# Performance work log

Measured on AMD Instinct MI355X. Metric: run time of the kernel, lower is better.

Reference implementation:

```python
import jax, jax.numpy as jnp
import numpy as np

D_MODEL = 1024
D_INNER = 2048   # expand * d_model
D_STATE = 16
DT_RANK = 64     # ceil(d_model / 16)
D_CONV = 4
L = 2048
EPS = 1e-5


def setup_inputs() -> dict:
    key = jax.random.key(0)
    ks = jax.random.split(key, 8)
    sc = lambda k, shape: jax.random.normal(k, shape, jnp.float32) * 0.02
    A = jnp.tile(jnp.arange(1, D_STATE + 1, dtype=jnp.float32), (D_INNER, 1))
    return {
        "x": jax.random.normal(ks[0], (L, D_MODEL), jnp.float32),
        "W_in": sc(ks[1], (D_MODEL, 2 * D_INNER)),          # in_proj (no bias)
        "W_conv": sc(ks[2], (D_CONV, D_INNER)),             # depthwise conv kernel
        "b_conv": jnp.zeros((D_INNER,), jnp.float32),
        "W_x": sc(ks[3], (D_INNER, DT_RANK + 2 * D_STATE)), # x_proj (no bias)
        "W_dt": sc(ks[4], (DT_RANK, D_INNER)),
        "b_dt": jnp.zeros((D_INNER,), jnp.float32),
        "A_log": jnp.log(A),
        "D": jnp.ones((D_INNER,), jnp.float32),
        "W_out": sc(ks[5], (D_INNER, D_MODEL)),             # out_proj (no bias)
        "ln_scale": jnp.ones((D_MODEL,), jnp.float32),
        "ln_bias": jnp.zeros((D_MODEL,), jnp.float32),
        "drop_key": 0,  # unused: training=False -> DropPath is identity
    }


def reference(x, W_in, W_conv, b_conv, W_x, W_dt, b_dt, A_log, D, W_out,
              ln_scale, ln_bias, drop_key):
    l = x.shape[0]
    # LayerNorm (flax default: mean/var over features)
    mu = jnp.mean(x, axis=-1, keepdims=True)
    var = jnp.mean(jnp.square(x), axis=-1, keepdims=True) - jnp.square(mu)
    xn = (x - mu) * jax.lax.rsqrt(var + EPS) * ln_scale + ln_bias

    # MambaBlock
    xr = xn @ W_in                         # (l, 2*d_inner)
    u, res = xr[:, :D_INNER], xr[:, D_INNER:]

    # causal depthwise conv: pad left d_conv-1, take first l outputs
    up = jnp.pad(u, ((D_CONV - 1, 0), (0, 0)))
    uc = b_conv + sum(up[k:k + l] * W_conv[k] for k in range(D_CONV))
    u2 = jax.nn.silu(uc)                   # (l, d_inner)

    # SSM params (input-dependent)
    x_dbl = u2 @ W_x                       # (l, dt_rank + 2n)
    dt = x_dbl[:, :DT_RANK]
    B = x_dbl[:, DT_RANK:DT_RANK + D_STATE]
    C = x_dbl[:, DT_RANK + D_STATE:]
    delta = jax.nn.softplus(dt @ W_dt + b_dt)   # (l, d_inner)
    A = -jnp.exp(A_log)                         # (d_inner, n)

    dA = jnp.exp(jnp.einsum('ld,dn->ldn', delta, A))   # (l, d_inner, n)
    dBu = jnp.einsum('ld,ln->ldn', delta * u2, B)       # (l, d_inner, n)

    def step(h, inp):
        dA_t, dBu_t, C_t = inp
        h = dA_t * h + dBu_t               # (d_inner, n)
        return h, h @ C_t                  # y_t: (d_inner,)

    h0 = jnp.zeros((D_INNER, D_STATE), dtype=u2.dtype)
    _, ys = jax.lax.scan(step, h0, (dA, dBu, C))
    y = ys + u2 * D                        # (l, d_inner)

    y = y * jax.nn.silu(res)
    out = y @ W_out                        # (l, d_model)
    return out + x                         # residual (DropPath identity in eval)
```

## Files before the change

### kernel.cpp

```cpp
#include <hip/hip_runtime.h>
#include <math.h>

#define L_SEQ 2048
#define DM 1024
#define DI 2048
#define DS 16
#define DTR 64
#define EPS 1e-5f
#define NSEG 16
#define SEGLEN 128

typedef float f32x4 __attribute__((ext_vector_type(4)));
typedef __bf16 bf16x8 __attribute__((ext_vector_type(8)));
typedef _Float16 h16x2 __attribute__((ext_vector_type(2)));

static __device__ __forceinline__ unsigned short f2bf(float f) {
  union { float f; unsigned u; } v; v.f = f;
  unsigned r = v.u + 0x7fffu + ((v.u >> 16) & 1u);
  return (unsigned short)(r >> 16);
}
static __device__ __forceinline__ float bf2f(unsigned short s) {
  union { unsigned u; float f; } v; v.u = ((unsigned)s) << 16;
  return v.f;
}

static __device__ __forceinline__ void gload16(const void* g, void* l) {
  __builtin_amdgcn_global_load_lds(
      (__attribute__((address_space(1))) void*)(unsigned long long)(g),
      (__attribute__((address_space(3))) void*)(unsigned)(unsigned long long)(l),
      16, 0, 0);
}

__global__ __launch_bounds__(256) void ln_kernel(const float* __restrict__ x,
                                                 const float* __restrict__ sc,
                                                 const float* __restrict__ bi,
                                                 unsigned short* __restrict__ xnb) {
  int row = blockIdx.x;
  int t = threadIdx.x;
  float4 xv = ((const float4*)(x + (size_t)row * DM))[t];
  float s  = xv.x + xv.y + xv.z + xv.w;
  float s2 = xv.x*xv.x + xv.y*xv.y + xv.z*xv.z + xv.w*xv.w;
  #pragma unroll
  for (int m = 32; m >= 1; m >>= 1) {
    s  += __shfl_xor(s, m);
    s2 += __shfl_xor(s2, m);
  }
  __shared__ float red[8];
  int wid = t >> 6, lane = t & 63;
  if (lane == 0) { red[wid] = s; red[4 + wid] = s2; }
  __syncthreads();
  s  = red[0] + red[1] + red[2] + red[3];
  s2 = red[4] + red[5] + red[6] + red[7];
  float mu = s * (1.f / DM);
  float var = s2 * (1.f / DM) - mu * mu;
  float rs = rsqrtf(var + EPS);
  float4 sc4 = ((const float4*)sc)[t];
  float4 bi4 = ((const float4*)bi)[t];
  ushort4 ob;
  ob.x = f2bf((xv.x - mu) * rs * sc4.x + bi4.x);
  ob.y = f2bf((xv.y - mu) * rs * sc4.y + bi4.y);
  ob.z = f2bf((xv.z - mu) * rs * sc4.z + bi4.z);
  ob.w = f2bf((xv.w - mu) * rs * sc4.w + bi4.w);
  *(ushort4*)&xnb[(size_t)row * DM + t * 4] = ob;
}

__global__ __launch_bounds__(256) void trans_bf16(
    const float* __restrict__ W, unsigned short* __restrict__ Wt, int K, int N)
{
  __shared__ unsigned short s[64][80];
  int n0 = blockIdx.x * 64, k0 = blockIdx.y * 64;
  int tid = threadIdx.x;
  #pragma unroll
  for (int p = 0; p < 4; ++p) {
    int i = p * 16 + (tid >> 4);
    int j = (tid & 15) * 4;
    float4 w = *(const float4*)&W[(size_t)(k0 + i) * N + n0 + j];
    s[j + 0][i] = f2bf(w.x); s[j + 1][i] = f2bf(w.y);
    s[j + 2][i] = f2bf(w.z); s[j + 3][i] = f2bf(w.w);
  }
  __syncthreads();
  #pragma unroll
  for (int q = 0; q < 2; ++q) {
    int n = q * 32 + (tid >> 3);
    int i8 = (tid & 7) * 8;
    *(int4*)&Wt[(size_t)(n0 + n) * K + k0 + i8] = *(const int4*)&s[n][i8];
  }
}

__global__ __launch_bounds__(256) void transpose_b16(
    const unsigned short* __restrict__ in, unsigned short* __restrict__ out,
    int R, int C)
{
  __shared__ unsigned short s[64][72];
  int c0 = blockIdx.x * 64, r0 = blockIdx.y * 64;
  int tid = threadIdx.x;
  #pragma unroll
  for (int p = 0; p < 2; ++p) {
    int r = p * 32 + (tid >> 3);
    int c = (tid & 7) * 8;
    *(int4*)&s[r][c] = *(const int4*)&in[(size_t)(r0 + r) * C + c0 + c];
  }
  __syncthreads();
  #pragma unroll
  for (int p = 0; p < 2; ++p) {
    int c = p * 32 + (tid >> 3);
    int r = (tid & 7) * 8;
    ushort4 a, b;
    a.x = s[r + 0][c]; a.y = s[r + 1][c]; a.z = s[r + 2][c]; a.w = s[r + 3][c];
    b.x = s[r + 4][c]; b.y = s[r + 5][c]; b.z = s[r + 6][c]; b.w = s[r + 7][c];
    *(ushort4*)&out[(size_t)(c0 + c) * R + r0 + r] = a;
    *(ushort4*)&out[(size_t)(c0 + c) * R + r0 + r + 4] = b;
  }
}

__global__ __launch_bounds__(256) void trans_wx(
    const float* __restrict__ Wx, unsigned short* __restrict__ Wxt)
{
  int i = blockIdx.x * 256 + threadIdx.x;
  int n = i >> 11, k = i & 2047;
  Wxt[i] = (n < 96) ? f2bf(Wx[(size_t)k * 96 + n]) : (unsigned short)0;
}

template<int BM, int BN, int EPI, int OUTB, int SPLITK>
__global__ __launch_bounds__(256) void gemm2(
    const unsigned short* __restrict__ A, int lda,
    const unsigned short* __restrict__ Bt, int ldb,
    void* __restrict__ Cv, int ldc,
    int M, int N, int K,
    const float* __restrict__ bias)
{
  constexpr int WM = BM / 2, WN = BN / 2;
  constexpr int FM = WM / 16, FN = WN / 16;
  __shared__ __align__(16) unsigned short smA[BM * 64];
  __shared__ __align__(16) unsigned short smB[BN * 64];

  int nwg = gridDim.x * gridDim.y;
  int bid = blockIdx.y * gridDim.x + blockIdx.x;
  if ((nwg & 7) == 0) {
    int cpx = nwg >> 3;
    bid = (bid & 7) * cpx + (bid >> 3);
  }
  int bx = bid % gridDim.x;
  int by = bid / gridDim.x;
  int m0 = by * BM, n0 = bx * BN;

  int tid = threadIdx.x;
  int lane = tid & 63, wid = tid >> 6;
  int wm = wid >> 1, wn = wid & 1;

  int kb = blockIdx.z * (K / SPLITK);
  int nt = (K / SPLITK) / 64;

  int rs = lane >> 3;
  int cs = (lane & 7) * 8;

  f32x4 acc[FM][FN];
  #pragma unroll
  for (int m = 0; m < FM; ++m)
    #pragma unroll
    for (int n = 0; n < FN; ++n) acc[m][n] = (f32x4){0.f, 0.f, 0.f, 0.f};

  for (int kt = 0; kt < nt; ++kt) {
    __syncthreads();
    #pragma unroll
    for (int i = 0; i < BM / 32; ++i) {
      int chunk = wid * (BM / 32) + i;
      gload16(A + (size_t)(m0 + chunk * 8 + rs) * lda + kb + kt * 64 + cs,
              (char*)smA + chunk * 1024);
    }
    #pragma unroll
    for (int i = 0; i < BN / 32; ++i) {
      int chunk = wid * (BN / 32) + i;
      gload16(Bt + (size_t)(n0 + chunk * 8 + rs) * ldb + kb + kt * 64 + cs,
              (char*)smB + chunk * 1024);
    }
    __syncthreads();

    #pragma unroll
    for (int kk = 0; kk < 2; ++kk) {
      bf16x8 aF[FM], bF[FN];
      #pragma unroll
      for (int m = 0; m < FM; ++m) {
        int r = wm * WM + m * 16 + (lane & 15);
        aF[m] = *(const bf16x8*)((const char*)smA + r * 128 + kk * 64 + (lane >> 4) * 16);
      }
      #pragma unroll
      for (int n = 0; n < FN; ++n) {
        int r = wn * WN + n * 16 + (lane & 15);
        bF[n] = *(const bf16x8*)((const char*)smB + r * 128 + kk * 64 + (lane >> 4) * 16);
      }
      #pragma unroll
      for (int m = 0; m < FM; ++m)
        #pragma unroll
        for (int n = 0; n < FN; ++n)
          acc[m][n] = __builtin_amdgcn_mfma_f32_16x16x32_bf16(
              aF[m], bF[n], acc[m][n], 0, 0, 0);
    }
  }

  float* Cf = (float*)Cv + (size_t)blockIdx.z * M * ldc;
  unsigned short* Cb = (unsigned short*)Cv;
  int cm = (lane >> 4) * 4, cn = lane & 15;
  #pragma unroll
  for (int m = 0; m < FM; ++m)
    #pragma unroll
    for (int n = 0; n < FN; ++n) {
      int col = n0 + wn * WN + n * 16 + cn;
      #pragma unroll
      for (int r = 0; r < 4; ++r) {
        int row = m0 + wm * WM + m * 16 + cm + r;
        float v = acc[m][n][r];
        if (EPI == 1) {
          float w = v + bias[row];
          v = (w > 20.f) ? w : log1pf(__expf(w));
        }
        if (OUTB) Cb[(size_t)row * ldc + col] = f2bf(v);
        else      Cf[(size_t)row * ldc + col] = v;
      }
    }
}

__global__ __launch_bounds__(256) void xdbl_reduce(
    const float* __restrict__ part, unsigned short* __restrict__ xdbl)
{
  int i = (blockIdx.x * 256 + threadIdx.x) * 4;
  const int SL = 2048 * 128;
  float4 s = *(const float4*)&part[i];
  #pragma unroll
  for (int z = 1; z < 16; ++z) {
    float4 p = *(const float4*)&part[(size_t)z * SL + i];
    s.x += p.x; s.y += p.y; s.z += p.z; s.w += p.w;
  }
  ushort4 ob;
  ob.x = f2bf(s.x); ob.y = f2bf(s.y); ob.z = f2bf(s.z); ob.w = f2bf(s.w);
  *(ushort4*)&xdbl[i] = ob;
}

__global__ __launch_bounds__(256) void out_reduce(
    const float* __restrict__ part, const float* __restrict__ x,
    float* __restrict__ out)
{
  int i = (blockIdx.x * 256 + threadIdx.x) * 4;
  const int SL = 2048 * 1024;
  float4 a = *(const float4*)&part[i];
  float4 b = *(const float4*)&part[SL + i];
  float4 r = *(const float4*)&x[i];
  float4 o;
  o.x = a.x + b.x + r.x; o.y = a.y + b.y + r.y;
  o.z = a.z + b.z + r.z; o.w = a.w + b.w + r.w;
  *(float4*)&out[i] = o;
}

__global__ __launch_bounds__(256) void conv_silu_kernel(
    const unsigned short* __restrict__ xrT,
    const float* __restrict__ Wc, const float* __restrict__ bc,
    unsigned short* __restrict__ u2T)
{
  int d = blockIdx.x;
  int l0 = blockIdx.y * 1024 + threadIdx.x * 4;
  const unsigned short* ur = xrT + (size_t)d * L_SEQ;
  float w0 = Wc[0 * DI + d], w1 = Wc[1 * DI + d];
  float w2 = Wc[2 * DI + d], w3 = Wc[3 * DI + d];
  float b = bc[d];
  ushort4 v0 = *(const ushort4*)&ur[l0];
  ushort4 vm; vm.x = vm.y = vm.z = vm.w = 0;
  if (l0 > 0) vm = *(const ushort4*)&ur[l0 - 4];
  float um3 = bf2f(vm.y), um2 = bf2f(vm.z), um1 = bf2f(vm.w);
  float x0 = bf2f(v0.x), x1 = bf2f(v0.y), x2 = bf2f(v0.z), x3 = bf2f(v0.w);
  float y0 = b + w0 * um3 + w1 * um2 + w2 * um1 + w3 * x0;
  float y1 = b + w0 * um2 + w1 * um1 + w2 * x0  + w3 * x1;
  float y2 = b + w0 * um1 + w1 * x0  + w2 * x1  + w3 * x2;
  float y3 = b + w0 * x0  + w1 * x1  + w2 * x2  + w3 * x3;
  ushort4 ob;
  ob.x = f2bf(y0 / (1.f + __expf(-y0)));
  ob.y = f2bf(y1 / (1.f + __expf(-y1)));
  ob.z = f2bf(y2 / (1.f + __expf(-y2)));
  ob.w = f2bf(y3 / (1.f + __expf(-y3)));
  *(ushort4*)&u2T[(size_t)d * L_SEQ + l0] = ob;
}


__global__ __launch_bounds__(128) void scan_pass1(
    const unsigned short* __restrict__ deltaT, const unsigned short* __restrict__ u2T,
    const unsigned short* __restrict__ xdbl,
    const float* __restrict__ A_log,
    float* __restrict__ hend, float* __restrict__ aprod)
{
  int t = threadIdx.x;
  int ch = t >> 4, n = t & 15;
  int li = (t & 15) * 4;
  int d0 = blockIdx.x * 8, d = d0 + ch;
  int s = blockIdx.y;
  int base = s * SEGLEN;

  __shared__ __align__(16) float sdT[8][68], suT[8][68], sBT[16][68];

  float An = -__expf(A_log[d * DS + n]);
  float h = 0.f, P = 1.f;

  ushort4 rdu, ru, rB[2];
  auto LOAD = [&](int c0) {
    rdu = *(const ushort4*)&deltaT[(size_t)d * L_SEQ + c0 + li];
    ru  = *(const ushort4*)&u2T[(size_t)d * L_SEQ + c0 + li];
    #pragma unroll
    for (int q = 0; q < 2; ++q) {
      int ll = c0 + (t >> 2) + q * 32;
      rB[q] = *(const ushort4*)&xdbl[(size_t)ll * 128 + 64 + (t & 3) * 4];
    }
  };

  LOAD(base);
  for (int cc = 0; cc < 2; ++cc) {
    __syncthreads();
    float d0v = bf2f(rdu.x), d1v = bf2f(rdu.y), d2v = bf2f(rdu.z), d3v = bf2f(rdu.w);
    sdT[ch][li + 0] = d0v; sdT[ch][li + 1] = d1v;
    sdT[ch][li + 2] = d2v; sdT[ch][li + 3] = d3v;
    suT[ch][li + 0] = d0v * bf2f(ru.x); suT[ch][li + 1] = d1v * bf2f(ru.y);
    suT[ch][li + 2] = d2v * bf2f(ru.z); suT[ch][li + 3] = d3v * bf2f(ru.w);
    #pragma unroll
    for (int q = 0; q < 2; ++q) {
      int ll = (t >> 2) + q * 32;
      int nb = (t & 3) * 4;
      sBT[nb + 0][ll] = bf2f(rB[q].x); sBT[nb + 1][ll] = bf2f(rB[q].y);
      sBT[nb + 2][ll] = bf2f(rB[q].z); sBT[nb + 3][ll] = bf2f(rB[q].w);
    }
    if (cc == 0) LOAD(base + 64);
    __syncthreads();

    #pragma unroll
    for (int g = 0; g < 64; g += 4) {
      float4 dl4 = *(const float4*)&sdT[ch][g];
      float4 du4 = *(const float4*)&suT[ch][g];
      float4 Bn4 = *(const float4*)&sBT[n][g];
      float dl[4] = {dl4.x, dl4.y, dl4.z, dl4.w};
      float du[4] = {du4.x, du4.y, du4.z, du4.w};
      float Bn[4] = {Bn4.x, Bn4.y, Bn4.z, Bn4.w};
      #pragma unroll
      for (int i = 0; i < 4; ++i) {
        float dA = __expf(dl[i] * An);
        P *= dA;
        h = dA * h + du[i] * Bn[i];
      }
    }
  }
  size_t idx = (size_t)s * (DI * DS) + d0 * DS + t;
  hend[idx]  = h;
  aprod[idx] = P;
}

__global__ __launch_bounds__(128) void scan_pass3(
    const unsigned short* __restrict__ deltaT, const unsigned short* __restrict__ u2T,
    const unsigned short* __restrict__ resT,
    const unsigned short* __restrict__ xdbl,
    const float* __restrict__ A_log, const float* __restrict__ Dp,
    const float* __restrict__ hend, const float* __restrict__ aprod,
    unsigned short* __restrict__ ybT)
{
  int t = threadIdx.x;
  int ch = t >> 4, n = t & 15;
  int li = (t & 15) * 4;
  int d0 = blockIdx.x * 8, d = d0 + ch;
  int s = blockIdx.y;
  int base = s * SEGLEN;

  __shared__ __align__(16) float sdT[8][68], suT[8][68];
  __shared__ __align__(16) float sBT[16][68], sCT[16][68];
  __shared__ __align__(4) _Float16 svh[64][134];

  float An = -__expf(A_log[d * DS + n]);

  float h = 0.f;
  int fi = d0 * DS + t;
  for (int k = 0; k < s; ++k)
    h = aprod[(size_t)k * (DI * DS) + fi] * h + hend[(size_t)k * (DI * DS) + fi];

  ushort4 rdu, ru, rB[2], rC[2];
  auto LOAD = [&](int c0) {
    rdu = *(const ushort4*)&deltaT[(size_t)d * L_SEQ + c0 + li];
    ru  = *(const ushort4*)&u2T[(size_t)d * L_SEQ + c0 + li];
    #pragma unroll
    for (int q = 0; q < 2; ++q) {
      int ll = c0 + (t >> 2) + q * 32;
      int n4 = (t & 3) * 4;
      rB[q] = *(const ushort4*)&xdbl[(size_t)ll * 128 + 64 + n4];
      rC[q] = *(const ushort4*)&xdbl[(size_t)ll * 128 + 80 + n4];
    }
  };

  LOAD(base);
  for (int cc = 0; cc < 2; ++cc) {
    int c0 = base + cc * 64;
    __syncthreads();
    float d0v = bf2f(rdu.x), d1v = bf2f(rdu.y), d2v = bf2f(rdu.z), d3v = bf2f(rdu.w);
    sdT[ch][li + 0] = d0v; sdT[ch][li + 1] = d1v;
    sdT[ch][li + 2] = d2v; sdT[ch][li + 3] = d3v;
    suT[ch][li + 0] = d0v * bf2f(ru.x); suT[ch][li + 1] = d1v * bf2f(ru.y);
    suT[ch][li + 2] = d2v * bf2f(ru.z); suT[ch][li + 3] = d3v * bf2f(ru.w);
    #pragma unroll
    for (int q = 0; q < 2; ++q) {
      int ll = (t >> 2) + q * 32;
      int nb = (t & 3) * 4;
      sBT[nb + 0][ll] = bf2f(rB[q].x); sBT[nb + 1][ll] = bf2f(rB[q].y);
      sBT[nb + 2][ll] = bf2f(rB[q].z); sBT[nb + 3][ll] = bf2f(rB[q].w);
      sCT[nb + 0][ll] = bf2f(rC[q].x); sCT[nb + 1][ll] = bf2f(rC[q].y);
      sCT[nb + 2][ll] = bf2f(rC[q].z); sCT[nb + 3][ll] = bf2f(rC[q].w);
    }
    if (cc == 0) LOAD(base + 64);
    __syncthreads();

    #pragma unroll
    for (int g = 0; g < 64; g += 4) {
      float4 dl4 = *(const float4*)&sdT[ch][g];
      float4 du4 = *(const float4*)&suT[ch][g];
      float4 Bn4 = *(const float4*)&sBT[n][g];
      float4 Cn4 = *(const float4*)&sCT[n][g];
      float dl[4] = {dl4.x, dl4.y, dl4.z, dl4.w};
      float du[4] = {du4.x, du4.y, du4.z, du4.w};
      float Bn[4] = {Bn4.x, Bn4.y, Bn4.z, Bn4.w};
      float Cn[4] = {Cn4.x, Cn4.y, Cn4.z, Cn4.w};
      #pragma unroll
      for (int i = 0; i < 4; ++i) {
        float dA = __expf(dl[i] * An);
        h = dA * h + du[i] * Bn[i];
        svh[g + i][t] = (_Float16)(h * Cn[i]);
      }
    }
    __syncthreads();

    #pragma unroll
    for (int r = 0; r < 4; ++r) {
      int idx = r * 128 + t;
      int ll = idx & 63, c2 = idx >> 6;
      const _Float16* row = &svh[ll][c2 * 16];
      float sum = 0.f;
      #pragma unroll
      for (int k = 0; k < 8; ++k) {
        h16x2 pv = *(const h16x2*)&row[k * 2];
        sum += (float)pv.x + (float)pv.y;
      }
      int dd = d0 + c2;
      float uv = bf2f(u2T[(size_t)dd * L_SEQ + c0 + ll]);
      float rv = bf2f(resT[(size_t)dd * L_SEQ + c0 + ll]);
      float sig = 1.f / (1.f + __expf(-rv));
      float yv = (sum + uv * Dp[dd]) * rv * sig;
      ybT[(size_t)dd * L_SEQ + c0 + ll] = f2bf(yv);
    }
  }
}

extern "C" void kernel_launch(void* const* d_in, const int* in_sizes, int n_in,
                              void* d_out, int out_size, void* d_ws, size_t ws_size,
                              hipStream_t stream)
{
  const float* x      = (const float*)d_in[0];
  const float* W_in   = (const float*)d_in[1];
  const float* W_conv = (const float*)d_in[2];
  const float* b_conv = (const float*)d_in[3];
  const float* W_x    = (const float*)d_in[4];
  const float* W_dt   = (const float*)d_in[5];
  const float* b_dt   = (const float*)d_in[6];
  const float* A_log  = (const float*)d_in[7];
  const float* Dp     = (const float*)d_in[8];
  const float* W_out  = (const float*)d_in[9];
  const float* ln_s   = (const float*)d_in[10];
  const float* ln_b   = (const float*)d_in[11];

  char* ws = (char*)d_ws;
  const size_t MB = 1u << 20;
  unsigned short* xnb    = (unsigned short*)(ws);
  unsigned short* xrT    = (unsigned short*)(ws + 4 * MB);
  unsigned short* u2T    = (unsigned short*)(ws + 20 * MB);
  unsigned short* u2b    = (unsigned short*)(ws + 28 * MB);
  float*          hend   = (float*)(ws + 28 * MB);
  float*          aprod  = (float*)(ws + 30 * MB);
  unsigned short* xdbl   = (unsigned short*)(ws + 36 * MB);
  unsigned short* Wxt    = (unsigned short*)(ws + 36 * MB + 512 * 1024);
  unsigned short* Wdt_t  = (unsigned short*)(ws + 37 * MB);
  unsigned short* deltaTb= (unsigned short*)(ws + 38 * MB);
  unsigned short* Wtin   = (unsigned short*)(ws + 38 * MB);
  float*          part   = (float*)(ws + 46 * MB);
  unsigned short* ybT    = (unsigned short*)(ws + 54 * MB);
  unsigned short* yb     = (unsigned short*)(ws + 4 * MB);
  unsigned short* Wtout  = xnb;
  const unsigned short* resT = xrT + (size_t)DI * L_SEQ;

  ln_kernel<<<L_SEQ, 256, 0, stream>>>(x, ln_s, ln_b, xnb);

  trans_bf16<<<dim3((2 * DI) / 64, DM / 64), 256, 0, stream>>>(W_in, Wtin, DM, 2 * DI);

  gemm2<64, 128, 0, 1, 1><<<dim3(L_SEQ / 128, (2 * DI) / 64), 256, 0, stream>>>(
      Wtin, DM, xnb, DM, xrT, L_SEQ, 2 * DI, L_SEQ, DM, nullptr);

  conv_silu_kernel<<<dim3(DI, 2), 256, 0, stream>>>(xrT, W_conv, b_conv, u2T);

  transpose_b16<<<dim3(L_SEQ / 64, DI / 64), 256, 0, stream>>>(u2T, u2b, DI, L_SEQ);

  trans_wx<<<(128 * 2048) / 256, 256, 0, stream>>>(W_x, Wxt);

  gemm2<64, 128, 0, 0, 16><<<dim3(1, L_SEQ / 64, 16), 256, 0, stream>>>(
      u2b, DI, Wxt, DI, part, 128, L_SEQ, 128, DI, nullptr);

  xdbl_reduce<<<(L_SEQ * 128) / 1024, 256, 0, stream>>>(part, xdbl);

  trans_bf16<<<dim3(DI / 64, DTR / 64), 256, 0, stream>>>(W_dt, Wdt_t, DTR, DI);

  gemm2<64, 128, 1, 1, 1><<<dim3(L_SEQ / 128, DI / 64), 256, 0, stream>>>(
      Wdt_t, DTR, xdbl, 128, deltaTb, L_SEQ, DI, L_SEQ, DTR, b_dt);

  trans_bf16<<<dim3(DM / 64, DI / 64), 256, 0, stream>>>(W_out, Wtout, DI, DM);

  scan_pass1<<<dim3(DI / 8, NSEG - 1), 128, 0, stream>>>(
      deltaTb, u2T, xdbl, A_log, hend, aprod);

  scan_pass3<<<dim3(DI / 8, NSEG), 128, 0, stream>>>(
      deltaTb, u2T, resT, xdbl, A_log, Dp, hend, aprod, ybT);

  transpose_b16<<<dim3(L_SEQ / 64, DI / 64), 256, 0, stream>>>(ybT, yb, DI, L_SEQ);

  gemm2<64, 64, 0, 0, 2><<<dim3(DM / 64, L_SEQ / 64, 2), 256, 0, stream>>>(
      yb, DI, Wtout, DI, part, DM, L_SEQ, DM, DI, nullptr);

  out_reduce<<<(L_SEQ * DM) / 1024, 256, 0, stream>>>(part, x, (float*)d_out);
}
```

Before: 185.2 us.

## Split selective scan into 32 segments with separate carry-prefix kernel

Halves the segment length of the chunked selective scan, from 128 to 64 timesteps, and doubles the segment count to 32. This shortens each block's serial recurrence and gives pass 1 and pass 3 twice as many blocks. The segment-carry combination moves out of pass 3, where every block looped over all earlier segments, into a new small scan_pass2 kernel that writes each segment's incoming state once. In exchange it adds a kernel launch, extra workspace for the per-segment initial states, and a short serial loop in pass2 over only 128 blocks.

```diff
diff --git a/kernel.cpp b/kernel.cpp
--- a/kernel.cpp
+++ b/kernel.cpp
@@ -7,8 +7,9 @@
 #define DS 16
 #define DTR 64
 #define EPS 1e-5f
-#define NSEG 16
-#define SEGLEN 128
+#define NSEG 32
+#define SEGLEN 64
+#define NSTATE (DI * DS)
 
 typedef float f32x4 __attribute__((ext_vector_type(4)));
 typedef __bf16 bf16x8 __attribute__((ext_vector_type(8)));
@@ -290,62 +291,67 @@
   int ch = t >> 4, n = t & 15;
   int li = (t & 15) * 4;
   int d0 = blockIdx.x * 8, d = d0 + ch;
-  int s = blockIdx.y;
-  int base = s * SEGLEN;
+  int base = blockIdx.y * SEGLEN;
 
   __shared__ __align__(16) float sdT[8][68], suT[8][68], sBT[16][68];
 
   float An = -__expf(A_log[d * DS + n]);
+
+  ushort4 rdu = *(const ushort4*)&deltaT[(size_t)d * L_SEQ + base + li];
+  ushort4 ru  = *(const ushort4*)&u2T[(size_t)d * L_SEQ + base + li];
+  ushort4 rB[2];
+  #pragma unroll
+  for (int q = 0; q < 2; ++q) {
+    int ll = base + (t >> 2) + q * 32;
+    rB[q] = *(const ushort4*)&xdbl[(size_t)ll * 128 + 64 + (t & 3) * 4];
+  }
+
+  float d0v = bf2f(rdu.x), d1v = bf2f(rdu.y), d2v = bf2f(rdu.z), d3v = bf2f(rdu.w);
+  sdT[ch][li + 0] = d0v; sdT[ch][li + 1] = d1v;
+  sdT[ch][li + 2] = d2v; sdT[ch][li + 3] = d3v;
+  suT[ch][li + 0] = d0v * bf2f(ru.x); suT[ch][li + 1] = d1v * bf2f(ru.y);
+  suT[ch][li + 2] = d2v * bf2f(ru.z); suT[ch][li + 3] = d3v * bf2f(ru.w);
+  #pragma unroll
+  for (int q = 0; q < 2; ++q) {
+    int ll = (t >> 2) + q * 32;
+    int nb = (t & 3) * 4;
+    sBT[nb + 0][ll] = bf2f(rB[q].x); sBT[nb + 1][ll] = bf2f(rB[q].y);
+    sBT[nb + 2][ll] = bf2f(rB[q].z); sBT[nb + 3][ll] = bf2f(rB[q].w);
+  }
+  __syncthreads();
+
   float h = 0.f, P = 1.f;
-
-  ushort4 rdu, ru, rB[2];
-  auto LOAD = [&](int c0) {
-    rdu = *(const ushort4*)&deltaT[(size_t)d * L_SEQ + c0 + li];
-    ru  = *(const ushort4*)&u2T[(size_t)d * L_SEQ + c0 + li];
-    #pragma unroll
-    for (int q = 0; q < 2; ++q) {
-      int ll = c0 + (t >> 2) + q * 32;
-      rB[q] = *(const ushort4*)&xdbl[(size_t)ll * 128 + 64 + (t & 3) * 4];
-    }
-  };
-
-  LOAD(base);
-  for (int cc = 0; cc < 2; ++cc) {
-    __syncthreads();
-    float d0v = bf2f(rdu.x), d1v = bf2f(rdu.y), d2v = bf2f(rdu.z), d3v = bf2f(rdu.w);
-    sdT[ch][li + 0] = d0v; sdT[ch][li + 1] = d1v;
-    sdT[ch][li + 2] = d2v; sdT[ch][li + 3] = d3v;
-    suT[ch][li + 0] = d0v * bf2f(ru.x); suT[ch][li + 1] = d1v * bf2f(ru.y);
-    suT[ch][li + 2] = d2v * bf2f(ru.z); suT[ch][li + 3] = d3v * bf2f(ru.w);
-    #pragma unroll
-    for (int q = 0; q < 2; ++q) {
-      int ll = (t >> 2) + q * 32;
-      int nb = (t & 3) * 4;
-      sBT[nb + 0][ll] = bf2f(rB[q].x); sBT[nb + 1][ll] = bf2f(rB[q].y);
-      sBT[nb + 2][ll] = bf2f(rB[q].z); sBT[nb + 3][ll] = bf2f(rB[q].w);
-    }
-    if (cc == 0) LOAD(base + 64);
-    __syncthreads();
-
-    #pragma unroll
-    for (int g = 0; g < 64; g += 4) {
-      float4 dl4 = *(const float4*)&sdT[ch][g];
-      float4 du4 = *(const float4*)&suT[ch][g];
-      float4 Bn4 = *(const float4*)&sBT[n][g];
-      float dl[4] = {dl4.x, dl4.y, dl4.z, dl4.w};
-      float du[4] = {du4.x, du4.y, du4.z, du4.w};
-      float Bn[4] = {Bn4.x, Bn4.y, Bn4.z, Bn4.w};
-      #pragma unroll
-      for (int i = 0; i < 4; ++i) {
-        float dA = __expf(dl[i] * An);
-        P *= dA;
-        h = dA * h + du[i] * Bn[i];
-      }
-    }
-  }
-  size_t idx = (size_t)s * (DI * DS) + d0 * DS + t;
+  #pragma unroll
+  for (int g = 0; g < 64; g += 4) {
+    float4 dl4 = *(const float4*)&sdT[ch][g];
+    float4 du4 = *(const float4*)&suT[ch][g];
+    float4 Bn4 = *(const float4*)&sBT[n][g];
+    float dl[4] = {dl4.x, dl4.y, dl4.z, dl4.w};
+    float du[4] = {du4.x, du4.y, du4.z, du4.w};
+    float Bn[4] = {Bn4.x, Bn4.y, Bn4.z, Bn4.w};
+    #pragma unroll
+    for (int i = 0; i < 4; ++i) {
+      float dA = __expf(dl[i] * An);
+      P *= dA;
+      h = dA * h + du[i] * Bn[i];
+    }
+  }
+  size_t idx = (size_t)blockIdx.y * NSTATE + d0 * DS + t;
   hend[idx]  = h;
   aprod[idx] = P;
+}
+
+__global__ __launch_bounds__(256) void scan_pass2(
+    const float* __restrict__ hend, const float* __restrict__ aprod,
+    float* __restrict__ h_in)
+{
+  int i = blockIdx.x * 256 + threadIdx.x;
+  float h = 0.f;
+  h_in[i] = 0.f;
+  for (int s = 0; s < NSEG - 1; ++s) {
+    h = aprod[(size_t)s * NSTATE + i] * h + hend[(size_t)s * NSTATE + i];
+    h_in[(size_t)(s + 1) * NSTATE + i] = h;
+  }
 }
 
 __global__ __launch_bounds__(128) void scan_pass3(
@@ -353,7 +359,7 @@
     const unsigned short* __restrict__ resT,
     const unsigned short* __restrict__ xdbl,
     const float* __restrict__ A_log, const float* __restrict__ Dp,
-    const float* __restrict__ hend, const float* __restrict__ aprod,
+    const float* __restrict__ h_in,
     unsigned short* __restrict__ ybT)
 {
   int t = threadIdx.x;
@@ -365,51 +371,43 @@
 
   __shared__ __align__(16) float sdT[8][68], suT[8][68];
   __shared__ __align__(16) float sBT[16][68], sCT[16][68];
-  __shared__ __align__(4) _Float16 svh[64][134];
+  __shared__ __align__(4) _Float16 svh[32][134];
 
   float An = -__expf(A_log[d * DS + n]);
-
-  float h = 0.f;
-  int fi = d0 * DS + t;
-  for (int k = 0; k < s; ++k)
-    h = aprod[(size_t)k * (DI * DS) + fi] * h + hend[(size_t)k * (DI * DS) + fi];
-
-  ushort4 rdu, ru, rB[2], rC[2];
-  auto LOAD = [&](int c0) {
-    rdu = *(const ushort4*)&deltaT[(size_t)d * L_SEQ + c0 + li];
-    ru  = *(const ushort4*)&u2T[(size_t)d * L_SEQ + c0 + li];
-    #pragma unroll
-    for (int q = 0; q < 2; ++q) {
-      int ll = c0 + (t >> 2) + q * 32;
-      int n4 = (t & 3) * 4;
-      rB[q] = *(const ushort4*)&xdbl[(size_t)ll * 128 + 64 + n4];
-      rC[q] = *(const ushort4*)&xdbl[(size_t)ll * 128 + 80 + n4];
-    }
-  };
-
-  LOAD(base);
-  for (int cc = 0; cc < 2; ++cc) {
-    int c0 = base + cc * 64;
-    __syncthreads();
-    float d0v = bf2f(rdu.x), d1v = bf2f(rdu.y), d2v = bf2f(rdu.z), d3v = bf2f(rdu.w);
-    sdT[ch][li + 0] = d0v; sdT[ch][li + 1] = d1v;
-    sdT[ch][li + 2] = d2v; sdT[ch][li + 3] = d3v;
-    suT[ch][li + 0] = d0v * bf2f(ru.x); suT[ch][li + 1] = d1v * bf2f(ru.y);
-    suT[ch][li + 2] = d2v * bf2f(ru.z); suT[ch][li + 3] = d3v * bf2f(ru.w);
-    #pragma unroll
-    for (int q = 0; q < 2; ++q) {
-      int ll = (t >> 2) + q * 32;
-      int nb = (t & 3) * 4;
-      sBT[nb + 0][ll] = bf2f(rB[q].x); sBT[nb + 1][ll] = bf2f(rB[q].y);
-      sBT[nb + 2][ll] = bf2f(rB[q].z); sBT[nb + 3][ll] = bf2f(rB[q].w);
-      sCT[nb + 0][ll] = bf2f(rC[q].x); sCT[nb + 1][ll] = bf2f(rC[q].y);
-      sCT[nb + 2][ll] = bf2f(rC[q].z); sCT[nb + 3][ll] = bf2f(rC[q].w);
-    }
-    if (cc == 0) LOAD(base + 64);
-    __syncthreads();
-
-    #pragma unroll
-    for (int g = 0; g < 64; g += 4) {
+  float h = h_in[(size_t)s * NSTATE + d0 * DS + t];
+
+  ushort4 rdu = *(const ushort4*)&deltaT[(size_t)d * L_SEQ + base + li];
+  ushort4 ru  = *(const ushort4*)&u2T[(size_t)d * L_SEQ + base + li];
+  ushort4 rB[2], rC[2];
+  #pragma unroll
+  for (int q = 0; q < 2; ++q) {
+    int ll = base + (t >> 2) + q * 32;
+    int n4 = (t & 3) * 4;
+    rB[q] = *(const ushort4*)&xdbl[(size_t)ll * 128 + 64 + n4];
+    rC[q] = *(const ushort4*)&xdbl[(size_t)ll * 128 + 80 + n4];
+  }
+
+  float d0v = bf2f(rdu.x), d1v = bf2f(rdu.y), d2v = bf2f(rdu.z), d3v = bf2f(rdu.w);
+  sdT[ch][li + 0] = d0v; sdT[ch][li + 1] = d1v;
+  sdT[ch][li + 2] = d2v; sdT[ch][li + 3] = d3v;
+  suT[ch][li + 0] = d0v * bf2f(ru.x); suT[ch][li + 1] = d1v * bf2f(ru.y);
+  suT[ch][li + 2] = d2v * bf2f(ru.z); suT[ch][li + 3] = d3v * bf2f(ru.w);
+  #pragma unroll
+  for (int q = 0; q < 2; ++q) {
+    int ll = (t >> 2) + q * 32;
+    int nb = (t & 3) * 4;
+    sBT[nb + 0][ll] = bf2f(rB[q].x); sBT[nb + 1][ll] = bf2f(rB[q].y);
+    sBT[nb + 2][ll] = bf2f(rB[q].z); sBT[nb + 3][ll] = bf2f(rB[q].w);
+    sCT[nb + 0][ll] = bf2f(rC[q].x); sCT[nb + 1][ll] = bf2f(rC[q].y);
+    sCT[nb + 2][ll] = bf2f(rC[q].z); sCT[nb + 3][ll] = bf2f(rC[q].w);
+  }
+  __syncthreads();
+
+  #pragma unroll
+  for (int half = 0; half < 2; ++half) {
+    int g0 = half * 32;
+    #pragma unroll
+    for (int g = g0; g < g0 + 32; g += 4) {
       float4 dl4 = *(const float4*)&sdT[ch][g];
       float4 du4 = *(const float4*)&suT[ch][g];
       float4 Bn4 = *(const float4*)&sBT[n][g];
@@ -422,15 +420,15 @@
       for (int i = 0; i < 4; ++i) {
         float dA = __expf(dl[i] * An);
         h = dA * h + du[i] * Bn[i];
-        svh[g + i][t] = (_Float16)(h * Cn[i]);
+        svh[g - g0 + i][t] = (_Float16)(h * Cn[i]);
       }
     }
     __syncthreads();
 
     #pragma unroll
-    for (int r = 0; r < 4; ++r) {
+    for (int r = 0; r < 2; ++r) {
       int idx = r * 128 + t;
-      int ll = idx & 63, c2 = idx >> 6;
+      int ll = idx & 31, c2 = idx >> 5;
       const _Float16* row = &svh[ll][c2 * 16];
       float sum = 0.f;
       #pragma unroll
@@ -439,12 +437,14 @@
         sum += (float)pv.x + (float)pv.y;
       }
       int dd = d0 + c2;
-      float uv = bf2f(u2T[(size_t)dd * L_SEQ + c0 + ll]);
-      float rv = bf2f(resT[(size_t)dd * L_SEQ + c0 + ll]);
+      int lg = base + g0 + ll;
+      float uv = bf2f(u2T[(size_t)dd * L_SEQ + lg]);
+      float rv = bf2f(resT[(size_t)dd * L_SEQ + lg]);
       float sig = 1.f / (1.f + __expf(-rv));
       float yv = (sum + uv * Dp[dd]) * rv * sig;
-      ybT[(size_t)dd * L_SEQ + c0 + ll] = f2bf(yv);
-    }
+      ybT[(size_t)dd * L_SEQ + lg] = f2bf(yv);
+    }
+    __syncthreads();
   }
 }
 
@@ -472,7 +472,7 @@
   unsigned short* u2T    = (unsigned short*)(ws + 20 * MB);
   unsigned short* u2b    = (unsigned short*)(ws + 28 * MB);
   float*          hend   = (float*)(ws + 28 * MB);
-  float*          aprod  = (float*)(ws + 30 * MB);
+  float*          aprod  = (float*)(ws + 32 * MB);
   unsigned short* xdbl   = (unsigned short*)(ws + 36 * MB);
   unsigned short* Wxt    = (unsigned short*)(ws + 36 * MB + 512 * 1024);
   unsigned short* Wdt_t  = (unsigned short*)(ws + 37 * MB);
@@ -480,6 +480,7 @@
   unsigned short* Wtin   = (unsigned short*)(ws + 38 * MB);
   float*          part   = (float*)(ws + 46 * MB);
   unsigned short* ybT    = (unsigned short*)(ws + 54 * MB);
+  float*          h_in   = (float*)(ws + 62 * MB);
   unsigned short* yb     = (unsigned short*)(ws + 4 * MB);
   unsigned short* Wtout  = xnb;
   const unsigned short* resT = xrT + (size_t)DI * L_SEQ;
@@ -512,8 +513,10 @@
   scan_pass1<<<dim3(DI / 8, NSEG - 1), 128, 0, stream>>>(
       deltaTb, u2T, xdbl, A_log, hend, aprod);
 
+  scan_pass2<<<NSTATE / 256, 256, 0, stream>>>(hend, aprod, h_in);
+
   scan_pass3<<<dim3(DI / 8, NSEG), 128, 0, stream>>>(
-      deltaTb, u2T, resT, xdbl, A_log, Dp, hend, aprod, ybT);
+      deltaTb, u2T, resT, xdbl, A_log, Dp, h_in, ybT);
 
   transpose_b16<<<dim3(L_SEQ / 64, DI / 64), 256, 0, stream>>>(ybT, yb, DI, L_SEQ);
 
```

Result: faster. 181.5 us (-2.0%).
